# Kernel tuning notes

Measured on AMD Instinct MI355X. Metric: run time of the kernel, lower is better.

Reference implementation:

```python
import jax, jax.numpy as jnp
import numpy as np

N = 65536      # conversation nodes (global vertex is node N)
D = 256        # hidden_dim
HEADS = 4
TOPK = 2
LN_EPS = 1e-5


def _ln(x, g, b):
    mu = jnp.mean(x, -1, keepdims=True)
    var = jnp.mean((x - mu) ** 2, -1, keepdims=True)
    return (x - mu) * jax.lax.rsqrt(var + LN_EPS) * g + b


def _moe(x, gate_W, gate_b, eW1, eb1, eg, ebt, eW2, eb2):
    # dense-compute-all-experts then top-k gather, exactly as the torch module
    w = jax.nn.softmax(x @ gate_W + gate_b, axis=-1)          # (N, E)
    tw, ti = jax.lax.top_k(w, TOPK)                            # (N, 2)
    tw = tw / jnp.sum(tw, -1, keepdims=True)
    h = jnp.einsum('nd,edh->neh', x, eW1) + eb1                # (N, E, D)
    h = jax.nn.gelu(_ln(h, eg, ebt), approximate=False)
    h = jnp.einsum('neh,eho->neo', h, eW2) + eb2
    sel = jnp.take_along_axis(h, ti[:, :, None], axis=1)      # (N, 2, D)
    return jnp.sum(sel * tw[:, :, None], axis=1)


def _gat(x, src, dst, W, a_s, a_d, bias, n):
    # PyG GATConv: per-head linear, additive attention, segment softmax over dst
    xw = (x @ W).reshape(n, HEADS, -1)                         # (n, H, D)
    e = jnp.sum(xw * a_s, -1)[src] + jnp.sum(xw * a_d, -1)[dst]  # (E, H)
    e = jnp.where(e > 0, e, 0.2 * e)                           # leaky_relu(0.2)
    m = jax.lax.stop_gradient(jax.ops.segment_max(e, dst, num_segments=n))
    p = jnp.exp(e - m[dst])
    z = jax.ops.segment_sum(p, dst, num_segments=n)
    alpha = p / (z[dst] + 1e-16)
    out = jax.ops.segment_sum(alpha[:, :, None] * xw[src], dst, num_segments=n)
    return out.reshape(n, -1) + bias


def _edges():
    # chain edges (i, i-1) for i in [2, N), star edges to/from global vertex N,
    # plus PyG default self-loops on all N+1 nodes
    s1 = np.arange(2, N, dtype=np.int64); d1 = s1 - 1
    g = np.arange(N, dtype=np.int64)
    sl = np.arange(N + 1, dtype=np.int64)
    src = np.concatenate([s1, np.full(N, N, np.int64), g, sl])
    dst = np.concatenate([d1, g, np.full(N, N, np.int64), sl])
    return src.astype(np.int32), dst.astype(np.int32)


def setup_inputs():
    key = jax.random.key(0)
    ks = iter(jax.random.split(key, 48))
    rn = lambda shape, s=0.02: jax.random.normal(next(ks), shape, jnp.float32) * s
    inp = {
        'feat_video': rn((N, 1024), 1.0),
        'feat_audio': rn((N, 512), 1.0),
        'feat_text': rn((N, 768), 1.0),
        'Wp_video': rn((1024, D)), 'bp_video': jnp.zeros((D,), jnp.float32),
        'Wp_audio': rn((512, D)), 'bp_audio': jnp.zeros((D,), jnp.float32),
        'Wp_text': rn((768, D)), 'bp_text': jnp.zeros((D,), jnp.float32),
        'mask_token': rn((D,), 1.0),
        'gate_W': rn((D, 8)), 'gate_b': jnp.zeros((8,), jnp.float32),
        'exp_W1': rn((8, D, D)), 'exp_b1': jnp.zeros((8, D), jnp.float32),
        'exp_g': jnp.ones((8, D), jnp.float32), 'exp_beta': jnp.zeros((8, D), jnp.float32),
        'exp_W2': rn((8, D, D)), 'exp_b2': jnp.zeros((8, D), jnp.float32),
        'global_vertex': rn((1, D), 1.0),
    }
    for l, ind in enumerate([D, HEADS * D, HEADS * D]):
        inp[f'gat_W{l}'] = rn((ind, HEADS * D))
        inp[f'gat_as{l}'] = rn((HEADS, D), 0.1)
        inp[f'gat_ad{l}'] = rn((HEADS, D), 0.1)
        inp[f'gat_b{l}'] = jnp.zeros((HEADS * D,), jnp.float32)
    # feature masking: int((N-1)*0.1) masked nodes, fixed permutation
    num_masked = int((N - 1) * 0.1)
    idx = jax.random.permutation(next(ks), N - 1)[:num_masked]
    inp['mask'] = jnp.zeros((N,), bool).at[idx].set(True)
    src, dst = _edges()
    inp['edge_src'] = jnp.asarray(src)
    inp['edge_dst'] = jnp.asarray(dst)
    return inp


def reference(feat_video, feat_audio, feat_text, Wp_video, bp_video, Wp_audio,
              bp_audio, Wp_text, bp_text, mask_token, gate_W, gate_b, exp_W1,
              exp_b1, exp_g, exp_beta, exp_W2, exp_b2, global_vertex,
              gat_W0, gat_as0, gat_ad0, gat_b0,
              gat_W1, gat_as1, gat_ad1, gat_b1,
              gat_W2, gat_as2, gat_ad2, gat_b2,
              mask, edge_src, edge_dst):
    # modal projection + mean over modals
    x = (feat_video @ Wp_video + bp_video
         + feat_audio @ Wp_audio + bp_audio
         + feat_text @ Wp_text + bp_text) / 3.0
    # feature masking with learned mask token
    x = jnp.where(mask[:, None], mask_token, x)
    # MoE alignment
    x = _moe(x, gate_W, gate_b, exp_W1, exp_b1, exp_g, exp_beta, exp_W2, exp_b2)
    # append global vertex, run 3 GATConv layers
    h = jnp.concatenate([x, global_vertex], axis=0)   # (N+1, D)
    n = N + 1
    h = _gat(h, edge_src, edge_dst, gat_W0, gat_as0, gat_ad0, gat_b0, n)
    h = _gat(h, edge_src, edge_dst, gat_W1, gat_as1, gat_ad1, gat_b1, n)
    h = _gat(h, edge_src, edge_dst, gat_W2, gat_as2, gat_ad2, gat_b2, n)
    # mean over heads -> final node embeddings (return_embeddings=True path)
    return h.reshape(n, HEADS, D).mean(axis=1)
```

## Files before the change

### kernel.cpp

```cpp
#include <hip/hip_runtime.h>
#include <math.h>

#define NV 65536
#define NT 65537
#define DMOD 256
#define DHID 1024
#define NEXPERT 8
#define CAPR (2*NV + NEXPERT*128)
#define EMX 262208

typedef __attribute__((ext_vector_type(4))) float f32x4;
typedef __attribute__((ext_vector_type(8))) short bf16x8;

static constexpr size_t kBig = (size_t)NT * DHID * sizeof(float);
static constexpr size_t oA   = 0;
static constexpr size_t oB   = kBig;
static constexpr size_t nf4  = (size_t)NT * 16;
static constexpr size_t oSS  = 2*kBig;
static constexpr size_t oSD  = oSS + nf4;
static constexpr size_t oZ   = oSD + nf4;
static constexpr size_t oP   = oZ + nf4;
static constexpr size_t oTW  = oP  + (size_t)EMX*16;
static constexpr size_t oTI  = oTW + (size_t)NV*8;
static constexpr size_t oPL  = oTI + (size_t)NV*8;
static constexpr size_t oPE  = oPL + (size_t)CAPR*4;
static constexpr size_t oPW  = oPE + (size_t)CAPR*4;
static constexpr size_t oDG  = oPW + (size_t)CAPR*4;
static constexpr size_t oOF  = oDG + (size_t)(NT+3)*4;
static constexpr size_t oCC  = oOF + (size_t)(NT+3)*4;
static constexpr size_t oCS  = oCC + (size_t)(NT+3)*4;
static constexpr size_t oCE  = oCS + (size_t)EMX*4;
static constexpr size_t oZS  = oCE + (size_t)EMX*4;
static constexpr size_t o9   = oZS + 256;
static constexpr size_t oBG  = o9  + 64;
static constexpr size_t oBO  = oBG + 256;
static constexpr size_t oMK  = oBO + 512;
static constexpr size_t oWC  = oMK + (size_t)NV*4;
static constexpr size_t oPBh = oWC + (size_t)8*2306*8;
static constexpr size_t zPB  = (size_t)256*2304*2;
static constexpr size_t oPBl = oPBh + zPB;
static constexpr size_t zG0  = (size_t)1024*256*2;
static constexpr size_t oG0h = oPBl + zPB;
static constexpr size_t oG0l = oG0h + zG0;
static constexpr size_t zG   = (size_t)1024*1024*2;
static constexpr size_t oG1h = oG0l + zG0;
static constexpr size_t oG1l = oG1h + zG;
static constexpr size_t oG2h = oG1l + zG;
static constexpr size_t oG2l = oG2h + zG;
static constexpr size_t zE   = (size_t)8*256*256*2;
static constexpr size_t oE1h = oG2l + zG;
static constexpr size_t oE1l = oE1h + zE;
static constexpr size_t oE2h = oE1l + zE;
static constexpr size_t oE2l = oE2h + zE;
static constexpr size_t WSNEED = oE2l + zE;

__device__ __forceinline__ unsigned f2bf(float f) {
  union { float f; unsigned u; } c; c.f = f;
  const unsigned u = c.u;
  return (u + 0x7FFFu + ((u >> 16) & 1u)) >> 16;
}
__device__ __forceinline__ float bf2f(unsigned h) {
  union { unsigned u; float f; } c; c.u = h << 16;
  return c.f;
}
__device__ __forceinline__ unsigned packsplit(float f) {
  const unsigned h = f2bf(f);
  const unsigned l = f2bf(f - bf2f(h));
  return (h << 16) | l;
}
__device__ __forceinline__ float unpk(unsigned u) {
  return bf2f(u >> 16) + bf2f(u & 0xFFFFu);
}
__device__ __forceinline__ void split8(const float4& v0, const float4& v1, uint4& uh, uint4& ul) {
  const float f[8] = {v0.x, v0.y, v0.z, v0.w, v1.x, v1.y, v1.z, v1.w};
  unsigned h[8], l[8];
  #pragma unroll
  for (int q = 0; q < 8; ++q) {
    h[q] = f2bf(f[q]);
    l[q] = f2bf(f[q] - bf2f(h[q]));
  }
  uh = make_uint4(h[0] | (h[1] << 16), h[2] | (h[3] << 16), h[4] | (h[5] << 16), h[6] | (h[7] << 16));
  ul = make_uint4(l[0] | (l[1] << 16), l[2] | (l[3] << 16), l[4] | (l[5] << 16), l[6] | (l[7] << 16));
}
__device__ __forceinline__ void unpack8(const uint4& u0, const uint4& u1, uint4& uh, uint4& ul) {
  uh.x = (u0.x >> 16) | (u0.y & 0xFFFF0000u);  ul.x = (u0.x & 0xFFFFu) | (u0.y << 16);
  uh.y = (u0.z >> 16) | (u0.w & 0xFFFF0000u);  ul.y = (u0.z & 0xFFFFu) | (u0.w << 16);
  uh.z = (u1.x >> 16) | (u1.y & 0xFFFF0000u);  ul.z = (u1.x & 0xFFFFu) | (u1.y << 16);
  uh.w = (u1.z >> 16) | (u1.w & 0xFFFF0000u);  ul.w = (u1.z & 0xFFFFu) | (u1.w << 16);
}

__global__ __launch_bounds__(256) void k_pack(float* __restrict__ buf, size_t n) {
  const size_t i = ((size_t)blockIdx.x * 256 + threadIdx.x) * 4;
  if (i >= n) return;
  float4 v = *(float4*)(buf + i);
  uint4 r;
  r.x = packsplit(v.x); r.y = packsplit(v.y); r.z = packsplit(v.z); r.w = packsplit(v.w);
  *(uint4*)(buf + i) = r;
}
__global__ __launch_bounds__(256) void k_pack_rows(float* __restrict__ hA,
                                                  const int* __restrict__ nbig,
                                                  const int* __restrict__ big) {
  const int nb = *nbig;
  for (int bi = blockIdx.x; bi < nb; bi += gridDim.x) {
    const int node = big[bi];
    float* row = hA + (size_t)node * DHID;
    for (int c = threadIdx.x; c < DHID; c += 256)
      ((unsigned*)row)[c] = packsplit(row[c]);
  }
}

__global__ __launch_bounds__(256) void k_tsplit(
    const float* __restrict__ in, int Kin, int Nin, int Kout, int koff,
    long ibstride, long obstride,
    unsigned short* __restrict__ oh, unsigned short* __restrict__ ol)
{
  __shared__ float t[64][68];
  const int b = blockIdx.z;
  in += (size_t)b * ibstride;
  oh += (size_t)b * obstride;
  ol += (size_t)b * obstride;
  const int k0 = blockIdx.x << 6, n0 = blockIdx.y << 6;
  const int tid = threadIdx.x;
  #pragma unroll
  for (int p = 0; p < 4; ++p) {
    const int r = (tid >> 4) + (p << 4);
    const int c4 = (tid & 15) << 2;
    *(float4*)&t[r][c4] = *(const float4*)(in + (size_t)(k0 + r) * Nin + n0 + c4);
  }
  __syncthreads();
  #pragma unroll
  for (int p = 0; p < 4; ++p) {
    const int n = n0 + (tid >> 4) + (p << 4);
    const int k4 = (tid & 15) << 2;
    unsigned h[4], l[4];
    #pragma unroll
    for (int q = 0; q < 4; ++q) {
      const float f = t[k4 + q][n - n0];
      h[q] = f2bf(f);
      l[q] = f2bf(f - bf2f(h[q]));
    }
    const int kg = koff + k0 + k4;
    const size_t off = ((size_t)(n >> 4) * (Kout >> 3) + (kg >> 3)) * 128 + (n & 15) * 8 + (kg & 7);
    *(uint2*)(oh + off) = make_uint2(h[0] | (h[1] << 16), h[2] | (h[3] << 16));
    *(uint2*)(ol + off) = make_uint2(l[0] | (l[1] << 16), l[2] | (l[3] << 16));
  }
}

template<int MODE>
__global__ __launch_bounds__(256) void gemm_m(
    int M, int K,
    const float* __restrict__ A0, int lda0,
    const float* __restrict__ A1, int lda1,
    const float* __restrict__ A2, int lda2,
    const unsigned short* __restrict__ BTh, const unsigned short* __restrict__ BTl,
    long bstride,
    float* __restrict__ C, int ldc,
    const float* __restrict__ bias0,
    const int* __restrict__ mask, const float* __restrict__ mtok,
    const float* __restrict__ biasx1, const float* __restrict__ biasx2,
    const int* __restrict__ plist, const int* __restrict__ pexp, const float* __restrict__ ptw,
    const float* __restrict__ gsrc)
{
  __shared__ uint4 AshF[2][512];
  __shared__ uint4 AslF[2][512];
  const int tid = threadIdx.x;
  int bn0, bm0;
  if (MODE == 0) {
    const int b = blockIdx.x;
    const int t = (b & 7) * 513 + (b >> 3);
    bn0 = (t & 7) << 7;
    bm0 = (t >> 3) << 7;
  } else {
    bn0 = blockIdx.x << 7;
    bm0 = blockIdx.y << 7;
  }
  int eb = 0;
  if (MODE == 2 || MODE == 3) eb = pexp[bm0];
  const int wid = tid >> 6, lane = tid & 63;
  const int wm = wid >> 1, wn = wid & 1;
  const int l15 = lane & 15, lg = lane >> 4;
  f32x4 acc[4][4];
  #pragma unroll
  for (int i = 0; i < 4; ++i)
    #pragma unroll
    for (int j = 0; j < 4; ++j) acc[i][j] = (f32x4)0.f;

  const int srow = tid >> 2;
  const int lgw  = tid & 3;
  const int k8 = lgw << 3;
  const size_t nfrow = (size_t)K * 2;
  const uint4* bph = (const uint4*)(BTh + (size_t)eb * bstride)
                     + (size_t)((bn0 >> 4) + (wn << 2)) * nfrow + lane;
  const uint4* bpl = (const uint4*)(BTl + (size_t)eb * bstride)
                     + (size_t)((bn0 >> 4) + (wn << 2)) * nfrow + lane;
  const int ridx = lane ^ lg;
  int nodes[2] = {0, 0};
  if (MODE == 2) {
    nodes[0] = plist[bm0 + srow];
    nodes[1] = plist[bm0 + srow + 64];
  }
  const int nkt = K >> 5;
  uint4 su0[2], su1[2];
  float4 sv0[2], sv1[2];

  auto loadA = [&](int kt) {
    const int kk = (kt << 5) + k8;
    #pragma unroll
    for (int p = 0; p < 2; ++p) {
      const int grow = bm0 + srow + (p << 6);
      if (MODE == 1) {
        const float* ap; int kloc;
        if (kk < 1024)      { ap = A0 + (size_t)grow * lda0; kloc = kk; }
        else if (kk < 1536) { ap = A1 + (size_t)grow * lda1; kloc = kk - 1024; }
        else                { ap = A2 + (size_t)grow * lda2; kloc = kk - 1536; }
        sv0[p] = *(const float4*)(ap + kloc);
        sv1[p] = *(const float4*)(ap + kloc + 4);
      } else if (MODE == 2) {
        const int nd = nodes[p];
        su0[p] = make_uint4(0, 0, 0, 0); su1[p] = su0[p];
        if (nd >= 0) {
          const unsigned* ap = (const unsigned*)gsrc + (size_t)nd * DMOD + kk;
          su0[p] = *(const uint4*)ap; su1[p] = *(const uint4*)(ap + 4);
        }
      } else {
        su0[p] = make_uint4(0, 0, 0, 0); su1[p] = su0[p];
        if (MODE == 3 || grow < M) {
          const unsigned* ap = (const unsigned*)A0 + (size_t)grow * lda0 + kk;
          su0[p] = *(const uint4*)ap; su1[p] = *(const uint4*)(ap + 4);
        }
      }
    }
  };
  auto storeA = [&](int buf) {
    #pragma unroll
    for (int p = 0; p < 2; ++p) {
      uint4 uh, ul;
      if (MODE == 1) split8(sv0[p], sv1[p], uh, ul);
      else           unpack8(su0[p], su1[p], uh, ul);
      const int r = srow + (p << 6);
      const int wi = ((r >> 4) << 6) + (lgw << 4) + ((r & 15) ^ lgw);
      AshF[buf][wi] = uh;
      AslF[buf][wi] = ul;
    }
  };

  loadA(0);
  storeA(0);
  __syncthreads();
  for (int kt = 0; kt < nkt; ++kt) {
    const int cur = kt & 1;
    bf16x8 bh[4], bl[4];
    #pragma unroll
    for (int j = 0; j < 4; ++j) {
      bh[j] = *(const bf16x8*)(bph + (size_t)j * nfrow + (kt << 6));
      bl[j] = *(const bf16x8*)(bpl + (size_t)j * nfrow + (kt << 6));
    }
    bf16x8 ah[4], al[4];
    #pragma unroll
    for (int i = 0; i < 4; ++i) {
      ah[i] = ((const bf16x8*)AshF[cur])[(((wm << 2) + i) << 6) + ridx];
      al[i] = ((const bf16x8*)AslF[cur])[(((wm << 2) + i) << 6) + ridx];
    }
    if (kt + 1 < nkt) loadA(kt + 1);
    #pragma unroll
    for (int i = 0; i < 4; ++i)
      #pragma unroll
      for (int j = 0; j < 4; ++j) {
        f32x4 t = acc[i][j];
        t = __builtin_amdgcn_mfma_f32_16x16x32_bf16(al[i], bh[j], t, 0, 0, 0);
        t = __builtin_amdgcn_mfma_f32_16x16x32_bf16(ah[i], bl[j], t, 0, 0, 0);
        t = __builtin_amdgcn_mfma_f32_16x16x32_bf16(ah[i], bh[j], t, 0, 0, 0);
        acc[i][j] = t;
      }
    if (kt + 1 < nkt) storeA(cur ^ 1);
    __syncthreads();
  }
  const int r0 = bm0 + (wm << 6), c0 = bn0 + (wn << 6);
  #pragma unroll
  for (int i = 0; i < 4; ++i) {
    #pragma unroll
    for (int v = 0; v < 4; ++v) {
      const int r = r0 + (i << 4) + (lg << 2) + v;
      if ((MODE == 0) && r >= M) continue;
      int node = 0; float pw = 0.f; int msk = 0;
      if (MODE == 3) { node = plist[r]; if (node < 0) continue; pw = ptw[r]; }
      if (MODE == 1) msk = mask[r];
      #pragma unroll
      for (int j = 0; j < 4; ++j) {
        const int c = c0 + (j << 4) + l15;
        const float a = acc[i][j][v];
        if (MODE == 0) {
          C[(size_t)r * ldc + c] = a;
        } else if (MODE == 1) {
          float val = (a + bias0[c] + biasx1[c] + biasx2[c]) * (1.f / 3.f);
          if (msk) val = mtok[c];
          ((unsigned*)C)[(size_t)r * ldc + c] = packsplit(val);
        } else if (MODE == 2) {
          C[(size_t)r * ldc + c] = a + bias0[eb * DMOD + c];
        } else {
          atomicAdd(C + (size_t)node * DMOD + c, (a + bias0[eb * DMOD + c]) * pw);
        }
      }
    }
  }
}

__global__ void k_mask_flag(const unsigned int* __restrict__ mw, int* __restrict__ flag) {
  const int i = blockIdx.x * 256 + threadIdx.x;
  if (i < 16384 && (mw[i] & 0xFFFFFF00u)) atomicOr(flag, 1);
}
__global__ void k_mask_canon(const void* __restrict__ m, const int* __restrict__ flag, int* __restrict__ out) {
  const int i = blockIdx.x * 256 + threadIdx.x;
  if (i >= NV) return;
  out[i] = (*flag) ? (int)((const unsigned char*)m)[i] : ((const int*)m)[i];
}

__global__ __launch_bounds__(64) void k_wc(
    const float* __restrict__ Wv, const float* __restrict__ Wa, const float* __restrict__ Wt,
    const float* __restrict__ bv, const float* __restrict__ ba, const float* __restrict__ bt,
    const float* __restrict__ mtok, const float* __restrict__ gW, const float* __restrict__ gb,
    double* __restrict__ Wc)
{
  const int r = blockIdx.x;
  const int l = threadIdx.x;
  float4 w;
  if (r < 1024)       w = *(const float4*)(Wv + (size_t)r * DMOD + l * 4);
  else if (r < 1536)  w = *(const float4*)(Wa + (size_t)(r - 1024) * DMOD + l * 4);
  else if (r < 2304)  w = *(const float4*)(Wt + (size_t)(r - 1536) * DMOD + l * 4);
  else if (r == 2304) {
    const float4 b0 = *(const float4*)(bv + l * 4);
    const float4 b1 = *(const float4*)(ba + l * 4);
    const float4 b2 = *(const float4*)(bt + l * 4);
    w = make_float4(b0.x + b1.x + b2.x, b0.y + b1.y + b2.y, b0.z + b1.z + b2.z, b0.w + b1.w + b2.w);
  } else              w = *(const float4*)(mtok + l * 4);
  const float wq[4] = {w.x, w.y, w.z, w.w};
  double acc[NEXPERT];
  #pragma unroll
  for (int e = 0; e < NEXPERT; ++e) acc[e] = 0.0;
  #pragma unroll
  for (int q = 0; q < 4; ++q) {
    const int d = l * 4 + q;
    #pragma unroll
    for (int e = 0; e < NEXPERT; ++e)
      acc[e] += (double)wq[q] * (double)gW[d * NEXPERT + e];
  }
  #pragma unroll
  for (int e = 0; e < NEXPERT; ++e) {
    #pragma unroll
    for (int o = 32; o > 0; o >>= 1) acc[e] += __shfl_xor(acc[e], o);
  }
  if (l == 0) {
    const double s = (r <= 2304) ? (1.0 / 3.0) : 1.0;
    #pragma unroll
    for (int e = 0; e < NEXPERT; ++e) {
      double v = acc[e] * s;
      if (r >= 2304) v += (double)gb[e];
      Wc[(size_t)e * 2306 + r] = v;
    }
  }
}

__global__ __launch_bounds__(256) void k_gate(
    const float* __restrict__ fv, const float* __restrict__ fa, const float* __restrict__ ft,
    const double* __restrict__ Wc, const int* __restrict__ mask,
    float* __restrict__ tw, int* __restrict__ ti, int* __restrict__ counts)
{
  __shared__ float  Af[64][64];
  __shared__ double Ws[64][8];
  __shared__ double Lg[64][8];
  __shared__ int    cnt[8];
  const int tid = threadIdx.x;
  const int nbase = blockIdx.x << 6;
  const int n = tid & 63;
  const int ep = tid >> 6;
  if (tid < 8) cnt[tid] = 0;
  double a0 = 0.0, a1 = 0.0;
  for (int c = 0; c < 36; ++c) {
    const int k0 = c << 6;
    {
      const int kq = ep << 4;
      const int kg = k0 + kq;
      const float* base; int kloc;
      if (kg < 1024)      { base = fv + (size_t)(nbase + n) * 1024; kloc = kg; }
      else if (kg < 1536) { base = fa + (size_t)(nbase + n) * 512;  kloc = kg - 1024; }
      else                { base = ft + (size_t)(nbase + n) * 768;  kloc = kg - 1536; }
      #pragma unroll
      for (int q = 0; q < 4; ++q) {
        const float4 f = *(const float4*)(base + kloc + q * 4);
        Af[kq + q * 4 + 0][n] = f.x;
        Af[kq + q * 4 + 1][n] = f.y;
        Af[kq + q * 4 + 2][n] = f.z;
        Af[kq + q * 4 + 3][n] = f.w;
      }
    }
    if (tid < 128) {
      const int e = tid >> 4;
      const int kk = (tid & 15) << 2;
      const double2 w01 = *(const double2*)(Wc + (size_t)e * 2306 + k0 + kk);
      const double2 w23 = *(const double2*)(Wc + (size_t)e * 2306 + k0 + kk + 2);
      Ws[kk + 0][e] = w01.x; Ws[kk + 1][e] = w01.y;
      Ws[kk + 2][e] = w23.x; Ws[kk + 3][e] = w23.y;
    }
    __syncthreads();
    #pragma unroll
    for (int k = 0; k < 64; ++k) {
      const double f = (double)Af[k][n];
      const double2 w = *(const double2*)&Ws[k][ep << 1];
      a0 += f * w.x;
      a1 += f * w.y;
    }
    __syncthreads();
  }
  Lg[n][(ep << 1) + 0] = a0;
  Lg[n][(ep << 1) + 1] = a1;
  __syncthreads();
  if (tid < 64) {
    const int node = nbase + tid;
    const int msk = mask[node];
    double le[NEXPERT];
    #pragma unroll
    for (int e = 0; e < NEXPERT; ++e)
      le[e] = msk ? Wc[(size_t)e * 2306 + 2305] : (Lg[tid][e] + Wc[(size_t)e * 2306 + 2304]);
    int b0 = -1, b1 = -1;
    double v0 = -1e300, v1 = -1e300;
    for (int e = 0; e < NEXPERT; ++e) {
      if (le[e] > v0) { v1 = v0; b1 = b0; v0 = le[e]; b0 = e; }
      else if (le[e] > v1) { v1 = le[e]; b1 = e; }
    }
    const double w0 = 1.0 / (1.0 + exp(v1 - v0));
    tw[node * 2 + 0] = (float)w0;
    tw[node * 2 + 1] = (float)(1.0 - w0);
    ti[node * 2 + 0] = b0;
    ti[node * 2 + 1] = b1;
    atomicAdd(&cnt[b0], 1);
    atomicAdd(&cnt[b1], 1);
  }
  __syncthreads();
  if (tid < 8 && cnt[tid] > 0) atomicAdd(&counts[tid], cnt[tid]);
}

__global__ void k_moe_offs(const int* __restrict__ counts, int* __restrict__ offs9) {
  if (threadIdx.x == 0 && blockIdx.x == 0) {
    int o = 0;
    for (int e = 0; e < NEXPERT; ++e) { offs9[e] = o; o += (counts[e] + 127) & ~127; }
    offs9[NEXPERT] = o;
  }
}
__global__ void k_moe_fill(const int* __restrict__ offs9, int* __restrict__ plist, int* __restrict__ pexp) {
  const int r = blockIdx.x * 256 + threadIdx.x;
  if (r >= CAPR) return;
  int e = 0;
  while (e < NEXPERT - 1 && r >= offs9[e + 1]) ++e;
  pexp[r] = e;
  plist[r] = -1;
}
__global__ __launch_bounds__(256) void k_moe_scatter(
    const int* __restrict__ ti, const float* __restrict__ tw,
    const int* __restrict__ offs9, int* __restrict__ cnt2,
    int* __restrict__ plist, float* __restrict__ ptw) {
  __shared__ int lcnt[NEXPERT];
  __shared__ int lbase[NEXPERT];
  const int tid = threadIdx.x;
  const int n = blockIdx.x * 256 + tid;
  if (tid < NEXPERT) lcnt[tid] = 0;
  __syncthreads();
  const int e0 = ti[n * 2 + 0];
  const int e1 = ti[n * 2 + 1];
  const bool v0 = (unsigned)e0 < NEXPERT;
  const bool v1 = (unsigned)e1 < NEXPERT;
  int r0 = 0, r1 = 0;
  if (v0) r0 = atomicAdd(&lcnt[e0], 1);
  if (v1) r1 = atomicAdd(&lcnt[e1], 1);
  __syncthreads();
  if (tid < NEXPERT && lcnt[tid] > 0) lbase[tid] = atomicAdd(&cnt2[tid], lcnt[tid]);
  __syncthreads();
  if (v0) {
    const int pos = offs9[e0] + lbase[e0] + r0;
    if ((unsigned)pos < CAPR) { plist[pos] = n; ptw[pos] = tw[n * 2 + 0]; }
  }
  if (v1) {
    const int pos = offs9[e1] + lbase[e1] + r1;
    if ((unsigned)pos < CAPR) { plist[pos] = n; ptw[pos] = tw[n * 2 + 1]; }
  }
}

__global__ __launch_bounds__(256) void k_ln_gelu(
    float* __restrict__ h1, const int* __restrict__ plist, const int* __restrict__ pexp,
    const float* __restrict__ g, const float* __restrict__ beta)
{
  const int r = blockIdx.x;
  if (plist[r] < 0) return;
  const int e = pexp[r];
  const int t = threadIdx.x;
  __shared__ float red[4];
  __shared__ float bc;
  const float v = h1[(size_t)r * DMOD + t];
  float s = v;
  #pragma unroll
  for (int o = 32; o > 0; o >>= 1) s += __shfl_xor(s, o);
  if ((t & 63) == 0) red[t >> 6] = s;
  __syncthreads();
  if (t == 0) bc = (red[0] + red[1] + red[2] + red[3]) * (1.f / 256.f);
  __syncthreads();
  const float mu = bc;
  const float dv = v - mu;
  float s2 = dv * dv;
  #pragma unroll
  for (int o = 32; o > 0; o >>= 1) s2 += __shfl_xor(s2, o);
  __syncthreads();
  if ((t & 63) == 0) red[t >> 6] = s2;
  __syncthreads();
  if (t == 0) bc = (red[0] + red[1] + red[2] + red[3]) * (1.f / 256.f);
  __syncthreads();
  const float var = bc;
  const float y = dv * rsqrtf(var + 1e-5f) * g[e * DMOD + t] + beta[e * DMOD + t];
  const float gl = y * 0.5f * (1.f + erff(y * 0.70710678118654752f));
  ((unsigned*)h1)[(size_t)r * DMOD + t] = packsplit(gl);
}

__global__ void k_set_global(float* __restrict__ h0, const float* __restrict__ gv) {
  h0[(size_t)NV * DMOD + threadIdx.x] = gv[threadIdx.x];
}

__global__ __launch_bounds__(256) void k_attn_s(
    const float* __restrict__ xw, const float* __restrict__ aS, const float* __restrict__ aD,
    float* __restrict__ sS, float* __restrict__ sD)
{
  const int wv = (blockIdx.x * 256 + threadIdx.x) >> 6;
  const int lane = threadIdx.x & 63;
  if (wv >= NT) return;
  const int h = lane >> 4, j = lane & 15;
  const float* row = xw + (size_t)wv * DHID + h * DMOD + j * 16;
  const float* av = aS + h * DMOD + j * 16;
  const float* dv = aD + h * DMOD + j * 16;
  float ps = 0.f, pd = 0.f;
  #pragma unroll
  for (int q = 0; q < 16; q += 4) {
    const float4 xv = *(const float4*)(row + q);
    const float4 a4 = *(const float4*)(av + q);
    const float4 d4 = *(const float4*)(dv + q);
    ps += xv.x * a4.x + xv.y * a4.y + xv.z * a4.z + xv.w * a4.w;
    pd += xv.x * d4.x + xv.y * d4.y + xv.z * d4.z + xv.w * d4.w;
  }
  #pragma unroll
  for (int o = 1; o <= 8; o <<= 1) { ps += __shfl_xor(ps, o); pd += __shfl_xor(pd, o); }
  if (j == 0) { sS[(size_t)wv * 4 + h] = ps; sD[(size_t)wv * 4 + h] = pd; }
}

__global__ __launch_bounds__(256) void k_edge_z(
    const int* __restrict__ esrc, const int* __restrict__ edst,
    const float* __restrict__ sS, const float* __restrict__ sD,
    float* __restrict__ p, float* __restrict__ z, int E)
{
  const int i = blockIdx.x * 256 + threadIdx.x;
  const bool valid = i < E;
  const int ic = valid ? i : (E - 1);
  const int dst = edst[ic];
  const int src = esrc[ic];
  const float4 a = *(const float4*)(sS + (size_t)src * 4);
  const float4 b = *(const float4*)(sD + (size_t)dst * 4);
  float e4[4] = {a.x + b.x, a.y + b.y, a.z + b.z, a.w + b.w};
  float pv[4];
  #pragma unroll
  for (int h = 0; h < 4; ++h) {
    const float e = e4[h] > 0.f ? e4[h] : 0.2f * e4[h];
    pv[h] = expf(e);
  }
  if (valid) *(float4*)(p + (size_t)i * 4) = make_float4(pv[0], pv[1], pv[2], pv[3]);
  float c4[4];
  #pragma unroll
  for (int h = 0; h < 4; ++h) c4[h] = valid ? pv[h] : 0.f;
  const int d0 = __shfl(dst, 0);
  if (__all(dst == d0)) {
    #pragma unroll
    for (int h = 0; h < 4; ++h) {
      #pragma unroll
      for (int o = 1; o <= 32; o <<= 1) c4[h] += __shfl_xor(c4[h], o);
    }
    if ((threadIdx.x & 63) == 0) {
      #pragma unroll
      for (int h = 0; h < 4; ++h) atomicAdd(&z[(size_t)d0 * 4 + h], c4[h]);
    }
  } else if (valid) {
    #pragma unroll
    for (int h = 0; h < 4; ++h) atomicAdd(&z[(size_t)dst * 4 + h], c4[h]);
  }
}

__global__ void k_deg(const int* __restrict__ edst, int* __restrict__ deg, int E) {
  const int i = blockIdx.x * 256 + threadIdx.x;
  const bool valid = i < E;
  const int ic = valid ? i : (E - 1);
  const int d = edst[ic];
  const int d0 = __shfl(d, 0);
  if (__all(d == d0)) {
    const unsigned long long m = __ballot(valid);
    if ((threadIdx.x & 63) == 0) atomicAdd(&deg[d0], __popcll(m));
  } else if (valid) {
    atomicAdd(&deg[d], 1);
  }
}
__global__ __launch_bounds__(1024) void k_scan(const int* __restrict__ deg, int* __restrict__ offs) {
  __shared__ int part[1024];
  const int t = threadIdx.x;
  const int s0 = t * 65;
  int sum = 0;
  for (int j = 0; j < 65; ++j) { const int idx = s0 + j; if (idx < NT) sum += deg[idx]; }
  part[t] = sum;
  __syncthreads();
  for (int off = 1; off < 1024; off <<= 1) {
    const int v = (t >= off) ? part[t - off] : 0;
    __syncthreads();
    part[t] += v;
    __syncthreads();
  }
  int run = part[t] - sum;
  for (int j = 0; j < 65; ++j) {
    const int idx = s0 + j;
    if (idx < NT) { offs[idx] = run; run += deg[idx]; }
  }
  if (t == 1023) offs[NT] = part[1023];
}
__global__ void k_csr_scatter(const int* __restrict__ esrc, const int* __restrict__ edst,
                              const int* __restrict__ offs, int* __restrict__ ccnt,
                              int* __restrict__ csrc, int* __restrict__ ceid, int E) {
  const int i = blockIdx.x * 256 + threadIdx.x;
  const bool valid = i < E;
  const int ic = valid ? i : (E - 1);
  const int d = edst[ic];
  const int lane = threadIdx.x & 63;
  const int d0 = __shfl(d, 0);
  if (__all(d == d0)) {
    const unsigned long long m = __ballot(valid);
    int base = 0;
    if (lane == 0) base = atomicAdd(&ccnt[d0], __popcll(m));
    base = __shfl(base, 0);
    if (valid) {
      const int pos = offs[d0] + base + __popcll(m & ((1ull << lane) - 1ull));
      csrc[pos] = esrc[ic];
      ceid[pos] = ic;
    }
  } else if (valid) {
    const int pos = offs[d] + atomicAdd(&ccnt[d], 1);
    csrc[pos] = esrc[ic];
    ceid[pos] = ic;
  }
}
__global__ void k_biglist(const int* __restrict__ offs, int* __restrict__ nbig,
                          int* __restrict__ big, int* __restrict__ bigoff) {
  for (int d = threadIdx.x; d < NT; d += 256) {
    const int dg = offs[d + 1] - offs[d];
    if (dg > 64) {
      const int idx = atomicAdd(nbig, 1);
      if (idx < 64) big[idx] = d;
    }
  }
  __syncthreads();
  if (threadIdx.x == 0) {
    int nb = *nbig; if (nb > 64) nb = 64;
    *nbig = nb;
    int o = 0;
    for (int i = 0; i < nb; ++i) {
      bigoff[i] = o;
      const int d = big[i];
      o += (offs[d + 1] - offs[d] + 255) / 256;
    }
    bigoff[nb] = o;
    bigoff[65] = o;
  }
}

__global__ __launch_bounds__(256) void k_agg_small(
    const float* __restrict__ xw, const float* __restrict__ p, const float* __restrict__ z,
    const int* __restrict__ offs, const int* __restrict__ csrc, const int* __restrict__ ceid,
    const float* __restrict__ bias, float* __restrict__ out)
{
  const int d = blockIdx.x;
  const int cq = threadIdx.x << 2;
  const int o0 = offs[d], o1 = offs[d + 1];
  const float4 b4 = *(const float4*)(bias + cq);
  if (o1 - o0 > 64) {
    *(float4*)(out + (size_t)d * DHID + cq) = b4;
    return;
  }
  const int h = cq >> 8;
  const float zz = z[(size_t)d * 4 + h] + 1e-16f;
  float4 acc = make_float4(0.f, 0.f, 0.f, 0.f);
  for (int k = o0; k < o1; ++k) {
    const float pw = p[(size_t)ceid[k] * 4 + h];
    const float4 v = *(const float4*)(xw + (size_t)csrc[k] * DHID + cq);
    acc.x += pw * v.x; acc.y += pw * v.y; acc.z += pw * v.z; acc.w += pw * v.w;
  }
  uint4 r;
  r.x = packsplit(acc.x / zz + b4.x);
  r.y = packsplit(acc.y / zz + b4.y);
  r.z = packsplit(acc.z / zz + b4.z);
  r.w = packsplit(acc.w / zz + b4.w);
  *(uint4*)((unsigned*)out + (size_t)d * DHID + cq) = r;
}

__global__ __launch_bounds__(256) void k_agg_big(
    const float* __restrict__ xw, const float* __restrict__ p, const float* __restrict__ z,
    const int* __restrict__ offs, const int* __restrict__ csrc, const int* __restrict__ ceid,
    const int* __restrict__ nbig, const int* __restrict__ big, const int* __restrict__ bigoff,
    float* __restrict__ out)
{
  const int nb = *nbig;
  const int total = bigoff[65] * 4;
  for (int w = blockIdx.x; w < total; w += gridDim.x) {
    const int cg = w & 3;
    const int chunk = w >> 2;
    int bi = 0;
    while (bi + 1 < nb && bigoff[bi + 1] <= chunk) ++bi;
    const int node = big[bi];
    const int local = chunk - bigoff[bi];
    const int e0 = offs[node] + local * 256;
    int e1 = offs[node + 1];
    if (e1 > e0 + 256) e1 = e0 + 256;
    const int c = cg * 256 + threadIdx.x;
    float acc = 0.f;
    for (int k = e0; k < e1; ++k)
      acc += p[(size_t)ceid[k] * 4 + cg] * xw[(size_t)csrc[k] * DHID + c];
    const float zz = z[(size_t)node * 4 + cg] + 1e-16f;
    atomicAdd(&out[(size_t)node * DHID + c], acc / zz);
  }
}

__global__ void k_head_mean(const float* __restrict__ h, float* __restrict__ out) {
  const size_t gid = (size_t)blockIdx.x * 256 + threadIdx.x;
  if (gid >= (size_t)NT * DMOD) return;
  const int n = (int)(gid >> 8);
  const int d = (int)(gid & 255);
  const unsigned* r = (const unsigned*)h + (size_t)n * DHID + d;
  out[gid] = (unpk(r[0]) + unpk(r[256]) + unpk(r[512]) + unpk(r[768])) * 0.25f;
}

__global__ void k_sentinel(float* out) { out[0] = 12345.0f; }

extern "C" void kernel_launch(void* const* d_in, const int* in_sizes, int n_in,
                              void* d_out, int out_size, void* d_ws, size_t ws_size,
                              hipStream_t stream) {
  const float* fv  = (const float*)d_in[0];
  const float* fa  = (const float*)d_in[1];
  const float* ft  = (const float*)d_in[2];
  const float* Wv  = (const float*)d_in[3];
  const float* bv  = (const float*)d_in[4];
  const float* Wa  = (const float*)d_in[5];
  const float* ba  = (const float*)d_in[6];
  const float* Wt  = (const float*)d_in[7];
  const float* bt  = (const float*)d_in[8];
  const float* mtok= (const float*)d_in[9];
  const float* gW  = (const float*)d_in[10];
  const float* gb  = (const float*)d_in[11];
  const float* eW1 = (const float*)d_in[12];
  const float* eb1 = (const float*)d_in[13];
  const float* eg  = (const float*)d_in[14];
  const float* ebt = (const float*)d_in[15];
  const float* eW2 = (const float*)d_in[16];
  const float* eb2 = (const float*)d_in[17];
  const float* gv  = (const float*)d_in[18];
  const float* gatW[3]  = {(const float*)d_in[19], (const float*)d_in[23], (const float*)d_in[27]};
  const float* gatAS[3] = {(const float*)d_in[20], (const float*)d_in[24], (const float*)d_in[28]};
  const float* gatAD[3] = {(const float*)d_in[21], (const float*)d_in[25], (const float*)d_in[29]};
  const float* gatB[3]  = {(const float*)d_in[22], (const float*)d_in[26], (const float*)d_in[30]};
  const void* maskraw = d_in[31];
  const int* esrc = (const int*)d_in[32];
  const int* edst = (const int*)d_in[33];
  const int E = in_sizes[32];

  if (ws_size < WSNEED) { k_sentinel<<<1, 1, 0, stream>>>((float*)d_out); return; }

  char* ws = (char*)d_ws;
  float* hA   = (float*)(ws + oA);
  float* hB   = (float*)(ws + oB);
  float* sS   = (float*)(ws + oSS);
  float* sD   = (float*)(ws + oSD);
  float* z    = (float*)(ws + oZ);
  float* p    = (float*)(ws + oP);
  float* tw   = (float*)(ws + oTW);
  int*   ti   = (int*)(ws + oTI);
  int*   plist= (int*)(ws + oPL);
  int*   pexp = (int*)(ws + oPE);
  float* ptw  = (float*)(ws + oPW);
  int*   deg  = (int*)(ws + oDG);
  int*   offs = (int*)(ws + oOF);
  int*   ccnt = (int*)(ws + oCC);
  int*   csrc = (int*)(ws + oCS);
  int*   ceid = (int*)(ws + oCE);
  int*   zsm  = (int*)(ws + oZS);
  int*   offs9= (int*)(ws + o9);
  int*   big  = (int*)(ws + oBG);
  int*   bigoff=(int*)(ws + oBO);
  int*   wsmask=(int*)(ws + oMK);
  double* Wc  = (double*)(ws + oWC);
  unsigned short* PBh = (unsigned short*)(ws + oPBh);
  unsigned short* PBl = (unsigned short*)(ws + oPBl);
  unsigned short* G0h = (unsigned short*)(ws + oG0h);
  unsigned short* G0l = (unsigned short*)(ws + oG0l);
  unsigned short* G1h = (unsigned short*)(ws + oG1h);
  unsigned short* G1l = (unsigned short*)(ws + oG1l);
  unsigned short* G2h = (unsigned short*)(ws + oG2h);
  unsigned short* G2l = (unsigned short*)(ws + oG2l);
  unsigned short* E1h = (unsigned short*)(ws + oE1h);
  unsigned short* E1l = (unsigned short*)(ws + oE1l);
  unsigned short* E2h = (unsigned short*)(ws + oE2h);
  unsigned short* E2l = (unsigned short*)(ws + oE2l);
  unsigned short* Gh[3] = {G0h, G1h, G2h};
  unsigned short* Gl_[3] = {G0l, G1l, G2l};
  float* x = (float*)d_out;

  const int eblk = (E + 255) / 256;

  hipMemsetAsync(zsm, 0, 256, stream);
  hipMemsetAsync(deg, 0, (size_t)(NT + 3) * 4, stream);
  hipMemsetAsync(ccnt, 0, (size_t)(NT + 3) * 4, stream);

  k_mask_flag<<<64, 256, 0, stream>>>((const unsigned int*)maskraw, zsm + 17);
  k_mask_canon<<<NV / 256, 256, 0, stream>>>(maskraw, zsm + 17, wsmask);

  k_tsplit<<<dim3(16, 4, 1), 256, 0, stream>>>(Wv, 1024, 256, 2304, 0,    0, 0, PBh, PBl);
  k_tsplit<<<dim3(8,  4, 1), 256, 0, stream>>>(Wa, 512,  256, 2304, 1024, 0, 0, PBh, PBl);
  k_tsplit<<<dim3(12, 4, 1), 256, 0, stream>>>(Wt, 768,  256, 2304, 1536, 0, 0, PBh, PBl);
  k_tsplit<<<dim3(4, 16, 1), 256, 0, stream>>>(gatW[0], 256, 1024, 256, 0, 0, 0, G0h, G0l);
  k_tsplit<<<dim3(16,16, 1), 256, 0, stream>>>(gatW[1], 1024, 1024, 1024, 0, 0, 0, G1h, G1l);
  k_tsplit<<<dim3(16,16, 1), 256, 0, stream>>>(gatW[2], 1024, 1024, 1024, 0, 0, 0, G2h, G2l);
  k_tsplit<<<dim3(4, 4, 8),  256, 0, stream>>>(eW1, 256, 256, 256, 0, 65536, 65536, E1h, E1l);
  k_tsplit<<<dim3(4, 4, 8),  256, 0, stream>>>(eW2, 256, 256, 256, 0, 65536, 65536, E2h, E2l);

  gemm_m<1><<<dim3(2, 512), 256, 0, stream>>>(
      NV, 2304, fv, 1024, fa, 512, ft, 768,
      PBh, PBl, 0, x, DMOD,
      bv, wsmask, mtok, ba, bt,
      nullptr, nullptr, nullptr, nullptr);

  k_wc<<<2306, 64, 0, stream>>>(Wv, Wa, Wt, bv, ba, bt, mtok, gW, gb, Wc);
  k_gate<<<NV / 64, 256, 0, stream>>>(fv, fa, ft, Wc, wsmask, tw, ti, zsm);
  k_moe_offs<<<1, 64, 0, stream>>>(zsm, offs9);
  k_moe_fill<<<CAPR / 256, 256, 0, stream>>>(offs9, plist, pexp);
  k_moe_scatter<<<NV / 256, 256, 0, stream>>>(ti, tw, offs9, zsm + 8, plist, ptw);
  gemm_m<2><<<dim3(2, CAPR / 128), 256, 0, stream>>>(
      CAPR, DMOD, nullptr, 0, nullptr, 0, nullptr, 0,
      E1h, E1l, (long)DMOD * DMOD, hB, DMOD,
      eb1, nullptr, nullptr, nullptr, nullptr,
      plist, pexp, nullptr, x);
  k_ln_gelu<<<CAPR, 256, 0, stream>>>(hB, plist, pexp, eg, ebt);
  hipMemsetAsync(hA, 0, (size_t)NT * DMOD * 4, stream);
  k_set_global<<<1, 256, 0, stream>>>(hA, gv);
  gemm_m<3><<<dim3(2, CAPR / 128), 256, 0, stream>>>(
      CAPR, DMOD, hB, DMOD, nullptr, 0, nullptr, 0,
      E2h, E2l, (long)DMOD * DMOD, hA, DMOD,
      eb2, nullptr, nullptr, nullptr, nullptr,
      plist, pexp, ptw, nullptr);
  k_pack<<<(int)(((size_t)NT * DMOD / 4 + 255) / 256), 256, 0, stream>>>(hA, (size_t)NT * DMOD);

  k_deg<<<eblk, 256, 0, stream>>>(edst, deg, E);
  k_scan<<<1, 1024, 0, stream>>>(deg, offs);
  k_csr_scatter<<<eblk, 256, 0, stream>>>(esrc, edst, offs, ccnt, csrc, ceid, E);
  k_biglist<<<1, 256, 0, stream>>>(offs, zsm + 16, big, bigoff);

  for (int l = 0; l < 3; ++l) {
    const int kin = (l == 0) ? DMOD : DHID;
    gemm_m<0><<<4104, 256, 0, stream>>>(
        NT, kin, hA, kin, nullptr, 0, nullptr, 0,
        Gh[l], Gl_[l], 0, hB, DHID,
        nullptr, nullptr, nullptr, nullptr, nullptr,
        nullptr, nullptr, nullptr, nullptr);
    k_attn_s<<<(NT + 3) / 4, 256, 0, stream>>>(hB, gatAS[l], gatAD[l], sS, sD);
    hipMemsetAsync(z, 0, nf4, stream);
    k_edge_z<<<eblk, 256, 0, stream>>>(esrc, edst, sS, sD, p, z, E);
    k_agg_small<<<NT, 256, 0, stream>>>(hB, p, z, offs, csrc, ceid, gatB[l], hA);
    k_agg_big<<<4096, 256, 0, stream>>>(hB, p, z, offs, csrc, ceid, zsm + 16, big, bigoff, hA);
    k_pack_rows<<<64, 256, 0, stream>>>(hA, zsm + 16, big);
  }

  k_head_mean<<<NT, 256, 0, stream>>>(hA, (float*)d_out);
}
```

Before: 3.506 ms.

## Compute MoE gate from projected features in fp32 with fp64 fallback for near-ties

Replaces the fp64 gate GEMM over the raw 2304-wide concatenated features with an fp32 dot product over the already projected 256-wide x, one wavefront per node. Nodes whose second and third logits fall within a small margin are flagged and recomputed in fp64 from the original features, so the top-2 expert selection is preserved. Expert counting moves to a separate kernel. The head-mean kernel is also vectorised to four elements per thread. The risk is that routing becomes sensitive to the tie threshold, and the gate now reads the bf16-split projected output rather than the raw inputs.

```diff
diff --git a/kernel.cpp b/kernel.cpp
--- a/kernel.cpp
+++ b/kernel.cpp
@@ -52,7 +52,9 @@
 static constexpr size_t oE1l = oE1h + zE;
 static constexpr size_t oE2h = oE1l + zE;
 static constexpr size_t oE2l = oE2h + zE;
-static constexpr size_t WSNEED = oE2l + zE;
+static constexpr size_t oFL  = oE2l + zE;
+static constexpr size_t oGWT = oFL + (size_t)NV*4;
+static constexpr size_t WSNEED = oGWT + (size_t)8*256*4;
 
 __device__ __forceinline__ unsigned f2bf(float f) {
   union { float f; unsigned u; } c; c.f = f;
@@ -360,83 +362,137 @@
   }
 }
 
-__global__ __launch_bounds__(256) void k_gate(
+__global__ void k_gwt(const float* __restrict__ gW, float* __restrict__ gWt) {
+  const int i = blockIdx.x * 256 + threadIdx.x;
+  if (i >= 8 * 256) return;
+  const int e = i >> 8, d = i & 255;
+  gWt[i] = gW[d * NEXPERT + e];
+}
+
+__global__ __launch_bounds__(256) void k_gate_f32(
+    const unsigned* __restrict__ xp, const float* __restrict__ gWt, const float* __restrict__ gb,
+    const double* __restrict__ Wc, const int* __restrict__ mask,
+    float* __restrict__ tw, int* __restrict__ ti,
+    int* __restrict__ flags, int* __restrict__ nflag)
+{
+  const int wv = (blockIdx.x * 256 + threadIdx.x) >> 6;
+  const int lane = threadIdx.x & 63;
+  if (wv >= NV) return;
+  const int msk = mask[wv];
+  float acc[NEXPERT];
+  #pragma unroll
+  for (int e = 0; e < NEXPERT; ++e) acc[e] = 0.f;
+  if (!msk) {
+    const uint4 u = *(const uint4*)(xp + (size_t)wv * DMOD + lane * 4);
+    const float xv[4] = {unpk(u.x), unpk(u.y), unpk(u.z), unpk(u.w)};
+    #pragma unroll
+    for (int e = 0; e < NEXPERT; ++e) {
+      const float4 w = *(const float4*)(gWt + e * DMOD + lane * 4);
+      acc[e] = xv[0] * w.x + xv[1] * w.y + xv[2] * w.z + xv[3] * w.w;
+    }
+    #pragma unroll
+    for (int e = 0; e < NEXPERT; ++e) {
+      #pragma unroll
+      for (int o = 32; o > 0; o >>= 1) acc[e] += __shfl_xor(acc[e], o);
+    }
+  }
+  if (lane == 0) {
+    float le[NEXPERT];
+    #pragma unroll
+    for (int e = 0; e < NEXPERT; ++e)
+      le[e] = msk ? (float)Wc[(size_t)e * 2306 + 2305] : (acc[e] + gb[e]);
+    int b0 = -1, b1 = -1;
+    float v0 = -1e30f, v1 = -1e30f, v2 = -1e30f;
+    #pragma unroll
+    for (int e = 0; e < NEXPERT; ++e) {
+      const float v = le[e];
+      if (v > v0)      { v2 = v1; v1 = v0; b1 = b0; v0 = v; b0 = e; }
+      else if (v > v1) { v2 = v1; v1 = v; b1 = e; }
+      else if (v > v2) { v2 = v; }
+    }
+    const double w0 = 1.0 / (1.0 + exp((double)v1 - (double)v0));
+    tw[wv * 2 + 0] = (float)w0;
+    tw[wv * 2 + 1] = (float)(1.0 - w0);
+    ti[wv * 2 + 0] = b0;
+    ti[wv * 2 + 1] = b1;
+    if (v1 - v2 < 1e-3f) {
+      const int idx = atomicAdd(nflag, 1);
+      if (idx < NV) flags[idx] = wv;
+    }
+  }
+}
+
+__global__ __launch_bounds__(256) void k_gate_fix(
     const float* __restrict__ fv, const float* __restrict__ fa, const float* __restrict__ ft,
     const double* __restrict__ Wc, const int* __restrict__ mask,
-    float* __restrict__ tw, int* __restrict__ ti, int* __restrict__ counts)
+    const int* __restrict__ flags, const int* __restrict__ nflag,
+    float* __restrict__ tw, int* __restrict__ ti)
 {
-  __shared__ float  Af[64][64];
-  __shared__ double Ws[64][8];
-  __shared__ double Lg[64][8];
-  __shared__ int    cnt[8];
+  int nf = *nflag; if (nf > NV) nf = NV;
+  const int lane = threadIdx.x & 63;
+  const int wix = (blockIdx.x * 256 + threadIdx.x) >> 6;
+  const int nw = gridDim.x * 4;
+  for (int idx = wix; idx < nf; idx += nw) {
+    const int node = flags[idx];
+    const int msk = mask[node];
+    double acc[NEXPERT];
+    #pragma unroll
+    for (int e = 0; e < NEXPERT; ++e) acc[e] = 0.0;
+    if (!msk) {
+      #pragma unroll
+      for (int c = 0; c < 9; ++c) {
+        const int kg0 = c * 256 + lane * 4;
+        const float* base; int kloc;
+        if (kg0 < 1024)      { base = fv + (size_t)node * 1024; kloc = kg0; }
+        else if (kg0 < 1536) { base = fa + (size_t)node * 512;  kloc = kg0 - 1024; }
+        else                 { base = ft + (size_t)node * 768;  kloc = kg0 - 1536; }
+        const float4 f = *(const float4*)(base + kloc);
+        const float fq[4] = {f.x, f.y, f.z, f.w};
+        #pragma unroll
+        for (int q = 0; q < 4; ++q) {
+          #pragma unroll
+          for (int e = 0; e < NEXPERT; ++e)
+            acc[e] += (double)fq[q] * Wc[(size_t)e * 2306 + kg0 + q];
+        }
+      }
+      #pragma unroll
+      for (int e = 0; e < NEXPERT; ++e) {
+        #pragma unroll
+        for (int o = 32; o > 0; o >>= 1) acc[e] += __shfl_xor(acc[e], o);
+      }
+    }
+    if (lane == 0) {
+      double le[NEXPERT];
+      #pragma unroll
+      for (int e = 0; e < NEXPERT; ++e)
+        le[e] = msk ? Wc[(size_t)e * 2306 + 2305] : (acc[e] + Wc[(size_t)e * 2306 + 2304]);
+      int b0 = -1, b1 = -1;
+      double v0 = -1e300, v1 = -1e300;
+      for (int e = 0; e < NEXPERT; ++e) {
+        if (le[e] > v0) { v1 = v0; b1 = b0; v0 = le[e]; b0 = e; }
+        else if (le[e] > v1) { v1 = le[e]; b1 = e; }
+      }
+      const double w0 = 1.0 / (1.0 + exp(v1 - v0));
+      tw[node * 2 + 0] = (float)w0;
+      tw[node * 2 + 1] = (float)(1.0 - w0);
+      ti[node * 2 + 0] = b0;
+      ti[node * 2 + 1] = b1;
+    }
+  }
+}
+
+__global__ __launch_bounds__(256) void k_count(const int* __restrict__ ti, int* __restrict__ counts) {
+  __shared__ int lcnt[NEXPERT];
   const int tid = threadIdx.x;
-  const int nbase = blockIdx.x << 6;
-  const int n = tid & 63;
-  const int ep = tid >> 6;
-  if (tid < 8) cnt[tid] = 0;
-  double a0 = 0.0, a1 = 0.0;
-  for (int c = 0; c < 36; ++c) {
-    const int k0 = c << 6;
-    {
-      const int kq = ep << 4;
-      const int kg = k0 + kq;
-      const float* base; int kloc;
-      if (kg < 1024)      { base = fv + (size_t)(nbase + n) * 1024; kloc = kg; }
-      else if (kg < 1536) { base = fa + (size_t)(nbase + n) * 512;  kloc = kg - 1024; }
-      else                { base = ft + (size_t)(nbase + n) * 768;  kloc = kg - 1536; }
-      #pragma unroll
-      for (int q = 0; q < 4; ++q) {
-        const float4 f = *(const float4*)(base + kloc + q * 4);
-        Af[kq + q * 4 + 0][n] = f.x;
-        Af[kq + q * 4 + 1][n] = f.y;
-        Af[kq + q * 4 + 2][n] = f.z;
-        Af[kq + q * 4 + 3][n] = f.w;
-      }
-    }
-    if (tid < 128) {
-      const int e = tid >> 4;
-      const int kk = (tid & 15) << 2;
-      const double2 w01 = *(const double2*)(Wc + (size_t)e * 2306 + k0 + kk);
-      const double2 w23 = *(const double2*)(Wc + (size_t)e * 2306 + k0 + kk + 2);
-      Ws[kk + 0][e] = w01.x; Ws[kk + 1][e] = w01.y;
-      Ws[kk + 2][e] = w23.x; Ws[kk + 3][e] = w23.y;
-    }
-    __syncthreads();
-    #pragma unroll
-    for (int k = 0; k < 64; ++k) {
-      const double f = (double)Af[k][n];
-      const double2 w = *(const double2*)&Ws[k][ep << 1];
-      a0 += f * w.x;
-      a1 += f * w.y;
-    }
-    __syncthreads();
-  }
-  Lg[n][(ep << 1) + 0] = a0;
-  Lg[n][(ep << 1) + 1] = a1;
-  __syncthreads();
-  if (tid < 64) {
-    const int node = nbase + tid;
-    const int msk = mask[node];
-    double le[NEXPERT];
-    #pragma unroll
-    for (int e = 0; e < NEXPERT; ++e)
-      le[e] = msk ? Wc[(size_t)e * 2306 + 2305] : (Lg[tid][e] + Wc[(size_t)e * 2306 + 2304]);
-    int b0 = -1, b1 = -1;
-    double v0 = -1e300, v1 = -1e300;
-    for (int e = 0; e < NEXPERT; ++e) {
-      if (le[e] > v0) { v1 = v0; b1 = b0; v0 = le[e]; b0 = e; }
-      else if (le[e] > v1) { v1 = le[e]; b1 = e; }
-    }
-    const double w0 = 1.0 / (1.0 + exp(v1 - v0));
-    tw[node * 2 + 0] = (float)w0;
-    tw[node * 2 + 1] = (float)(1.0 - w0);
-    ti[node * 2 + 0] = b0;
-    ti[node * 2 + 1] = b1;
-    atomicAdd(&cnt[b0], 1);
-    atomicAdd(&cnt[b1], 1);
-  }
-  __syncthreads();
-  if (tid < 8 && cnt[tid] > 0) atomicAdd(&counts[tid], cnt[tid]);
+  const int n = blockIdx.x * 256 + tid;
+  if (tid < NEXPERT) lcnt[tid] = 0;
+  __syncthreads();
+  const int e0 = ti[n * 2 + 0];
+  const int e1 = ti[n * 2 + 1];
+  if ((unsigned)e0 < NEXPERT) atomicAdd(&lcnt[e0], 1);
+  if ((unsigned)e1 < NEXPERT) atomicAdd(&lcnt[e1], 1);
+  __syncthreads();
+  if (tid < NEXPERT && lcnt[tid] > 0) atomicAdd(&counts[tid], lcnt[tid]);
 }
 
 __global__ void k_moe_offs(const int* __restrict__ counts, int* __restrict__ offs9) {
@@ -726,13 +782,22 @@
   }
 }
 
-__global__ void k_head_mean(const float* __restrict__ h, float* __restrict__ out) {
+__global__ __launch_bounds__(256) void k_head_mean(const float* __restrict__ h, float* __restrict__ out) {
   const size_t gid = (size_t)blockIdx.x * 256 + threadIdx.x;
-  if (gid >= (size_t)NT * DMOD) return;
-  const int n = (int)(gid >> 8);
-  const int d = (int)(gid & 255);
-  const unsigned* r = (const unsigned*)h + (size_t)n * DHID + d;
-  out[gid] = (unpk(r[0]) + unpk(r[256]) + unpk(r[512]) + unpk(r[768])) * 0.25f;
+  if (gid >= (size_t)NT * 64) return;
+  const int n = (int)(gid >> 6);
+  const int dq = (int)(gid & 63) << 2;
+  const unsigned* r = (const unsigned*)h + (size_t)n * DHID + dq;
+  const uint4 r0 = *(const uint4*)(r + 0);
+  const uint4 r1 = *(const uint4*)(r + 256);
+  const uint4 r2 = *(const uint4*)(r + 512);
+  const uint4 r3 = *(const uint4*)(r + 768);
+  float4 o;
+  o.x = (unpk(r0.x) + unpk(r1.x) + unpk(r2.x) + unpk(r3.x)) * 0.25f;
+  o.y = (unpk(r0.y) + unpk(r1.y) + unpk(r2.y) + unpk(r3.y)) * 0.25f;
+  o.z = (unpk(r0.z) + unpk(r1.z) + unpk(r2.z) + unpk(r3.z)) * 0.25f;
+  o.w = (unpk(r0.w) + unpk(r1.w) + unpk(r2.w) + unpk(r3.w)) * 0.25f;
+  *(float4*)(out + (size_t)n * DMOD + dq) = o;
 }
 
 __global__ void k_sentinel(float* out) { out[0] = 12345.0f; }
@@ -805,6 +870,8 @@
   unsigned short* E1l = (unsigned short*)(ws + oE1l);
   unsigned short* E2h = (unsigned short*)(ws + oE2h);
   unsigned short* E2l = (unsigned short*)(ws + oE2l);
+  int*   flags = (int*)(ws + oFL);
+  float* gWt   = (float*)(ws + oGWT);
   unsigned short* Gh[3] = {G0h, G1h, G2h};
   unsigned short* Gl_[3] = {G0l, G1l, G2l};
   float* x = (float*)d_out;
@@ -834,7 +901,11 @@
       nullptr, nullptr, nullptr, nullptr);
 
   k_wc<<<2306, 64, 0, stream>>>(Wv, Wa, Wt, bv, ba, bt, mtok, gW, gb, Wc);
-  k_gate<<<NV / 64, 256, 0, stream>>>(fv, fa, ft, Wc, wsmask, tw, ti, zsm);
+  k_gwt<<<8, 256, 0, stream>>>(gW, gWt);
+  k_gate_f32<<<NV / 4, 256, 0, stream>>>((const unsigned*)x, gWt, gb, Wc, wsmask,
+                                         tw, ti, flags, zsm + 18);
+  k_gate_fix<<<64, 256, 0, stream>>>(fv, fa, ft, Wc, wsmask, flags, zsm + 18, tw, ti);
+  k_count<<<NV / 256, 256, 0, stream>>>(ti, zsm);
   k_moe_offs<<<1, 64, 0, stream>>>(zsm, offs9);
   k_moe_fill<<<CAPR / 256, 256, 0, stream>>>(offs9, plist, pexp);
   k_moe_scatter<<<NV / 256, 256, 0, stream>>>(ti, tw, offs9, zsm + 8, plist, ptw);
@@ -873,5 +944,5 @@
     k_pack_rows<<<64, 256, 0, stream>>>(hA, zsm + 16, big);
   }
 
-  k_head_mean<<<NT, 256, 0, stream>>>(hA, (float*)d_out);
-}
+  k_head_mean<<<(int)(((size_t)NT * 64 + 255) / 256), 256, 0, stream>>>(hA, (float*)d_out);
+}
```

After: 3.404 ms (median of 2 runs). 2.9% less time.
